# Optimization experiments

Hardware: AMD Instinct MI355X
Metric: run time of the kernel (lower is better)

## Reference

```python
import jax, jax.numpy as jnp
import numpy as np
from math import sqrt

H = 8          # num_heads
ROPE_BASE = 10000.0


def _rotate_half_interleaved(t):
    # rearrange '... (dim r) -> r ... dim' with r=2 then stack [-x2, x1] back interleaved
    x1 = t[..., 0::2]
    x2 = t[..., 1::2]
    return jnp.stack([-x2, x1], axis=-1).reshape(t.shape)


def _apply_rope(t, pos):
    # t: [B,H,L,W] with W even; pos: [L]
    W = t.shape[-1]
    theta = 1.0 / (ROPE_BASE ** (jnp.arange(0, W, 2, dtype=jnp.float32) / W))  # [W/2]
    m_theta = pos[:, None].astype(jnp.float32) * theta[None, :]                 # [L,W/2]
    m_theta = jnp.repeat(m_theta, 2, axis=-1)                                   # [L,W]
    cos = jnp.cos(m_theta)
    sin = jnp.sin(m_theta)
    return cos * t + sin * _rotate_half_interleaved(t)


def setup_inputs() -> dict:
    key = jax.random.key(0)
    ks = jax.random.split(key, 7)
    B, L, D = 2, 2048, 512
    s = 0.05
    return {
        'x': jax.random.normal(ks[0], (B, L, D), jnp.float32),
        'Wq': jax.random.normal(ks[1], (D, D), jnp.float32) * s,
        'bq': jnp.zeros((D,), jnp.float32),
        'Wk': jax.random.normal(ks[2], (D, D), jnp.float32) * s,
        'bk': jnp.zeros((D,), jnp.float32),
        'Wv': jax.random.normal(ks[3], (D, D), jnp.float32) * s,
        'bv': jnp.zeros((D,), jnp.float32),
        'Wo': jax.random.normal(ks[4], (D, D), jnp.float32) * s,
        'bo': jnp.zeros((D,), jnp.float32),
        'bias_emb': jax.random.normal(ks[5], (2, H), jnp.float32) * s,
        'n_vars': 32,
        'n_tokens': 64,
    }


def reference(x, Wq, bq, Wk, bk, Wv, bv, Wo, bo, bias_emb, n_vars, n_tokens):
    B, L, D = x.shape
    E = D // H  # head_dim
    # q/k/v projections (nn.Linear: x @ W.T + b)
    q = (x @ Wq.T + bq).reshape(B, L, H, E).transpose(0, 2, 1, 3)  # [B,H,L,E]
    k = (x @ Wk.T + bk).reshape(B, L, H, E).transpose(0, 2, 1, 3)  # [B,H,L,E]
    v = (x @ Wv.T + bv).reshape(B, L, H, E)                        # [B,S,H,E]

    # partial RoPE on first half of head_dim (partial_factor=(0.0, 0.5))
    half = E // 2
    pos = jnp.arange(L)
    q = jnp.concatenate([_apply_rope(q[..., :half], pos), q[..., half:]], axis=-1)
    k = jnp.concatenate([_apply_rope(k[..., :half], pos), k[..., half:]], axis=-1)

    # binary attention bias by same-variable indicator
    idx = jnp.arange(L)
    vid = idx // n_tokens
    tid = idx % n_tokens
    same_var = vid[:, None] == vid[None, :]                         # [L,L]
    bias = jnp.where(same_var[None], bias_emb[1][:, None, None],
                     bias_emb[0][:, None, None])                    # [H,L,L]

    # TimerCovariateMask: allow same-variable causal; last n_tokens queries
    # may also attend to all earlier keys
    allowed = same_var & (tid[None, :] <= tid[:, None])
    last_rows = idx >= (L - n_tokens)
    early_cols = idx < (L - n_tokens)
    blocked = (~allowed) & ~(last_rows[:, None] & early_cols[None, :])
    attn_mask = jnp.where(blocked[None], -jnp.inf, bias)            # [H,L,L]

    scale = 1.0 / sqrt(E)
    scores = jnp.einsum('bhle,bhse->bhls', q, k) + attn_mask[None]  # [B,H,L,L]
    A = jax.nn.softmax(scale * scores, axis=-1)
    Vout = jnp.einsum('bhls,bshd->blhd', A, v)                      # [B,L,H,E]
    out = Vout.reshape(B, L, H * E) @ Wo.T + bo                     # [B,L,D]
    return out
```

## Files before the change

kernel.cpp:

```cpp
#include <hip/hip_runtime.h>

typedef __attribute__((ext_vector_type(8))) short short8;
typedef __attribute__((ext_vector_type(4))) float f32x4;
typedef __attribute__((ext_vector_type(4))) unsigned short u16x4;

#define MFMA16(a, b, c) __builtin_amdgcn_mfma_f32_16x16x32_bf16(a, b, c, 0, 0, 0)

#define GLD16(gp, lp) __builtin_amdgcn_global_load_lds( \
    (const __attribute__((address_space(1))) unsigned int*)(gp), \
    (__attribute__((address_space(3))) unsigned int*)(lp), 16, 0, 0)

__device__ __forceinline__ unsigned short f2bf(float f) {
    union { float f; unsigned int u; } v; v.f = f;
    unsigned int r = (v.u + 0x7fffu + ((v.u >> 16) & 1u)) >> 16;
    return (unsigned short)r;
}

__global__ __launch_bounds__(256) void convertk(
    const float* __restrict__ x, const float* __restrict__ wq,
    const float* __restrict__ wk, const float* __restrict__ wv,
    const float* __restrict__ wo, unsigned short* __restrict__ xb,
    unsigned short* __restrict__ wb)
{
    int i = (blockIdx.x * 256 + threadIdx.x) * 4;
    const float* src;
    unsigned short* dst;
    if (i < 2097152) { src = x + i; dst = xb + i; }
    else {
        int j = i - 2097152;
        int w = j >> 18;
        int o = j & 262143;
        src = (w == 0 ? wq : w == 1 ? wk : w == 2 ? wv : wo) + o;
        dst = wb + j;
    }
    float4 v = *(const float4*)src;
    u16x4 p;
    p[0] = f2bf(v.x); p[1] = f2bf(v.y); p[2] = f2bf(v.z); p[3] = f2bf(v.w);
    *(u16x4*)dst = p;
}

__global__ __launch_bounds__(256) void gemm_qkv(
    const unsigned short* __restrict__ xb, const unsigned short* __restrict__ wb,
    const float* __restrict__ bq, const float* __restrict__ bk,
    const float* __restrict__ bv,
    unsigned short* __restrict__ qb, unsigned short* __restrict__ kb,
    unsigned short* __restrict__ vT)
{
    const int z = blockIdx.z;
    const unsigned short* Wz = wb + z * 262144;
    const int n0 = blockIdx.x * 128, m0 = blockIdx.y * 64;
    __shared__ unsigned short Al[64 * 32];
    __shared__ unsigned short Bl[128 * 32];
    const int t = threadIdx.x;
    const int lane = t & 63, w = t >> 6;
    const int wrow = (w >> 1) * 32, wcol = (w & 1) * 64;
    const int quad = lane >> 4, n16 = lane & 15;
    const int rA = lane >> 2;
    const int cG = (((lane & 3) ^ ((rA >> 1) & 3))) * 8;
    const int slotq = (quad ^ ((n16 >> 1) & 3)) * 8;
    const int fragA0 = (wrow >> 4) * 512 + n16 * 32 + slotq;
    const int fragB0 = (wcol >> 4) * 512 + n16 * 32 + slotq;
    f32x4 acc[2][4] = {};
    for (int k0 = 0; k0 < 512; k0 += 32) {
        __syncthreads();
        GLD16(&xb[(m0 + w * 16 + rA) * 512 + k0 + cG],      &Al[(w * 16) * 32]);
        GLD16(&Wz[(n0 + w * 32 + rA) * 512 + k0 + cG],      &Bl[(w * 32) * 32]);
        GLD16(&Wz[(n0 + w * 32 + 16 + rA) * 512 + k0 + cG], &Bl[(w * 32 + 16) * 32]);
        __syncthreads();
        short8 af[2], bfr[4];
        #pragma unroll
        for (int i = 0; i < 2; i++) af[i]  = *(const short8*)&Al[fragA0 + i * 512];
        #pragma unroll
        for (int i = 0; i < 4; i++) bfr[i] = *(const short8*)&Bl[fragB0 + i * 512];
        #pragma unroll
        for (int mi = 0; mi < 2; mi++)
            #pragma unroll
            for (int ni = 0; ni < 4; ni++)
                acc[mi][ni] = MFMA16(af[mi], bfr[ni], acc[mi][ni]);
    }
    const float* bias_p = (z == 0) ? bq : (z == 1) ? bk : bv;
    unsigned short* dst01 = (z == 0) ? qb : kb;
    #pragma unroll
    for (int mi = 0; mi < 2; mi++) {
        #pragma unroll
        for (int ni = 0; ni < 4; ni++) {
            const int n = n0 + wcol + ni * 16 + n16;
            const int mb = m0 + wrow + mi * 16 + quad * 4;
            const float bias = bias_p[n];
            const int h = n >> 6;
            const int e_lo = ni * 16 + n16;
            f32x4 v = acc[mi][ni];
            if (z < 2) {
                float vr[4];
                #pragma unroll
                for (int r = 0; r < 4; r++) vr[r] = v[r] + bias;
                if (ni < 2) {
                    const int j = e_lo >> 1;
                    const float theta = exp2f(-(float)j * 0.8304820237218405f);
                    #pragma unroll
                    for (int r = 0; r < 4; r++) {
                        int l = (mb + r) & 2047;
                        float s, c;
                        __sincosf((float)l * theta, &s, &c);
                        float p = __shfl_xor(vr[r], 1);
                        vr[r] = (e_lo & 1) ? (c * vr[r] + s * p) : (c * vr[r] - s * p);
                    }
                }
                #pragma unroll
                for (int r = 0; r < 4; r++) {
                    int m = mb + r, b = m >> 11, l = m & 2047;
                    dst01[((b * 8 + h) * 2048 + l) * 64 + e_lo] = f2bf(vr[r]);
                }
            } else {
                int b = mb >> 11, l = mb & 2047;
                u16x4 pk;
                #pragma unroll
                for (int r = 0; r < 4; r++) pk[r] = f2bf(v[r] + bias);
                *(u16x4*)&vT[((b * 8 + h) * 64 + e_lo) * 2048 + l] = pk;
            }
        }
    }
}

__global__ __launch_bounds__(256) void attn_all(
    const unsigned short* __restrict__ qb, const unsigned short* __restrict__ kb,
    const unsigned short* __restrict__ vT, const float* __restrict__ bias_emb,
    unsigned short* __restrict__ voutb,
    float* __restrict__ Opart, float* __restrict__ Mp, float* __restrict__ Lp)
{
    const int xid = blockIdx.x, h = blockIdx.y, b = blockIdx.z;
    const int t = threadIdx.x, lane = t & 63, w = t >> 6;
    const int quad = lane >> 4, n16 = lane & 15;
    const int bh = b * 8 + h;
    __shared__ unsigned short Pl[4 * 1280];
    unsigned short* Pw = &Pl[w * 1280];
    const int qoff = bh * 2048 * 64;
    const float scale = 0.125f;
    const float bias_same = bias_emb[8 + h];
    const int iloc = w * 16 + quad * 4;

    if (xid < 31) {
        const int var = xid;
        const int m0 = var * 64 + w * 16;
        const int j0 = var * 64;
        short8 aq0 = *(const short8*)&qb[qoff + (m0 + n16) * 64 + quad * 8];
        short8 aq1 = *(const short8*)&qb[qoff + (m0 + n16) * 64 + 32 + quad * 8];
        f32x4 sc[4];
        #pragma unroll
        for (int nt = 0; nt < 4; nt++) {
            short8 k0f = *(const short8*)&kb[qoff + (j0 + nt * 16 + n16) * 64 + quad * 8];
            short8 k1f = *(const short8*)&kb[qoff + (j0 + nt * 16 + n16) * 64 + 32 + quad * 8];
            f32x4 s = {};
            s = MFMA16(aq0, k0f, s);
            s = MFMA16(aq1, k1f, s);
            sc[nt] = s;
        }
        float zl[4][4];
        #pragma unroll
        for (int nt = 0; nt < 4; nt++) {
            int jloc = nt * 16 + n16;
            #pragma unroll
            for (int r = 0; r < 4; r++) {
                float zz = scale * (sc[nt][r] + bias_same);
                if (jloc > iloc + r) zz = -1e30f;
                zl[nt][r] = zz;
            }
        }
        float cm[4], rsum[4], pr[4][4];
        #pragma unroll
        for (int r = 0; r < 4; r++)
            cm[r] = fmaxf(fmaxf(zl[0][r], zl[1][r]), fmaxf(zl[2][r], zl[3][r]));
        #pragma unroll
        for (int off = 1; off < 16; off <<= 1)
            #pragma unroll
            for (int r = 0; r < 4; r++)
                cm[r] = fmaxf(cm[r], __shfl_xor(cm[r], off));
        #pragma unroll
        for (int nt = 0; nt < 4; nt++)
            #pragma unroll
            for (int r = 0; r < 4; r++)
                pr[nt][r] = __expf(zl[nt][r] - cm[r]);
        #pragma unroll
        for (int r = 0; r < 4; r++)
            rsum[r] = (pr[0][r] + pr[1][r]) + (pr[2][r] + pr[3][r]);
        #pragma unroll
        for (int off = 1; off < 16; off <<= 1)
            #pragma unroll
            for (int r = 0; r < 4; r++)
                rsum[r] += __shfl_xor(rsum[r], off);
        #pragma unroll
        for (int nt = 0; nt < 4; nt++) {
            int s = nt >> 1, c = (nt & 1) * 16 + n16;
            #pragma unroll
            for (int r = 0; r < 4; r++)
                Pw[s * 640 + (quad * 4 + r) * 40 + c] = f2bf(pr[nt][r]);
        }
        short8 pa0 = *(const short8*)&Pw[0 * 640 + n16 * 40 + quad * 8];
        short8 pa1 = *(const short8*)&Pw[1 * 640 + n16 * 40 + quad * 8];
        f32x4 oacc[4] = {};
        #pragma unroll
        for (int et = 0; et < 4; et++) {
            const int vrow = (bh * 64 + et * 16 + n16) * 2048;
            short8 v0 = *(const short8*)&vT[vrow + j0 + quad * 8];
            short8 v1 = *(const short8*)&vT[vrow + j0 + 32 + quad * 8];
            oacc[et] = MFMA16(pa0, v0, oacc[et]);
            oacc[et] = MFMA16(pa1, v1, oacc[et]);
        }
        #pragma unroll
        for (int et = 0; et < 4; et++) {
            #pragma unroll
            for (int r = 0; r < 4; r++) {
                float o = oacc[et][r] / rsum[r];
                int l = m0 + quad * 4 + r;
                voutb[(b * 2048 + l) * 512 + h * 64 + et * 16 + n16] = f2bf(o);
            }
        }
    } else {
        const int split = xid - 31;
        const int m0 = 31 * 64 + w * 16;
        const float bias_diff = bias_emb[h];
        short8 aq0 = *(const short8*)&qb[qoff + (m0 + n16) * 64 + quad * 8];
        short8 aq1 = *(const short8*)&qb[qoff + (m0 + n16) * 64 + 32 + quad * 8];
        f32x4 oacc[4] = {};
        float mrow[4], lrow[4];
        #pragma unroll
        for (int r = 0; r < 4; r++) { mrow[r] = -1e30f; lrow[r] = 0.f; }
        #pragma unroll
        for (int ci = 0; ci < 4; ci++) {
            const int chunk = split * 4 + ci;
            const bool diag = (chunk == 31);
            const float biasv = diag ? bias_same : bias_diff;
            const int j0 = chunk * 64;
            f32x4 sc[4];
            #pragma unroll
            for (int nt = 0; nt < 4; nt++) {
                short8 k0f = *(const short8*)&kb[qoff + (j0 + nt * 16 + n16) * 64 + quad * 8];
                short8 k1f = *(const short8*)&kb[qoff + (j0 + nt * 16 + n16) * 64 + 32 + quad * 8];
                f32x4 s = {};
                s = MFMA16(aq0, k0f, s);
                s = MFMA16(aq1, k1f, s);
                sc[nt] = s;
            }
            float zl[4][4];
            #pragma unroll
            for (int nt = 0; nt < 4; nt++) {
                int jloc = nt * 16 + n16;
                #pragma unroll
                for (int r = 0; r < 4; r++) {
                    float zz = scale * (sc[nt][r] + biasv);
                    if (diag && jloc > iloc + r) zz = -1e30f;
                    zl[nt][r] = zz;
                }
            }
            float cm[4];
            #pragma unroll
            for (int r = 0; r < 4; r++)
                cm[r] = fmaxf(fmaxf(zl[0][r], zl[1][r]), fmaxf(zl[2][r], zl[3][r]));
            #pragma unroll
            for (int off = 1; off < 16; off <<= 1)
                #pragma unroll
                for (int r = 0; r < 4; r++)
                    cm[r] = fmaxf(cm[r], __shfl_xor(cm[r], off));
            float mnew[4], alpha[4], rsum[4], pr[4][4];
            #pragma unroll
            for (int r = 0; r < 4; r++) {
                mnew[r] = fmaxf(mrow[r], cm[r]);
                alpha[r] = __expf(mrow[r] - mnew[r]);
            }
            #pragma unroll
            for (int nt = 0; nt < 4; nt++)
                #pragma unroll
                for (int r = 0; r < 4; r++)
                    pr[nt][r] = __expf(zl[nt][r] - mnew[r]);
            #pragma unroll
            for (int r = 0; r < 4; r++)
                rsum[r] = (pr[0][r] + pr[1][r]) + (pr[2][r] + pr[3][r]);
            #pragma unroll
            for (int off = 1; off < 16; off <<= 1)
                #pragma unroll
                for (int r = 0; r < 4; r++)
                    rsum[r] += __shfl_xor(rsum[r], off);
            #pragma unroll
            for (int r = 0; r < 4; r++) {
                lrow[r] = lrow[r] * alpha[r] + rsum[r];
                mrow[r] = mnew[r];
            }
            #pragma unroll
            for (int et = 0; et < 4; et++)
                #pragma unroll
                for (int r = 0; r < 4; r++)
                    oacc[et][r] *= alpha[r];
            #pragma unroll
            for (int nt = 0; nt < 4; nt++) {
                int s = nt >> 1, c = (nt & 1) * 16 + n16;
                #pragma unroll
                for (int r = 0; r < 4; r++)
                    Pw[s * 640 + (quad * 4 + r) * 40 + c] = f2bf(pr[nt][r]);
            }
            short8 pa0 = *(const short8*)&Pw[0 * 640 + n16 * 40 + quad * 8];
            short8 pa1 = *(const short8*)&Pw[1 * 640 + n16 * 40 + quad * 8];
            #pragma unroll
            for (int et = 0; et < 4; et++) {
                const int vrow = (bh * 64 + et * 16 + n16) * 2048;
                short8 v0 = *(const short8*)&vT[vrow + j0 + quad * 8];
                short8 v1 = *(const short8*)&vT[vrow + j0 + 32 + quad * 8];
                oacc[et] = MFMA16(pa0, v0, oacc[et]);
                oacc[et] = MFMA16(pa1, v1, oacc[et]);
            }
        }
        const int pb = (bh * 8 + split) * 64;
        #pragma unroll
        for (int et = 0; et < 4; et++)
            #pragma unroll
            for (int r = 0; r < 4; r++)
                Opart[(pb + w * 16 + quad * 4 + r) * 64 + et * 16 + n16] = oacc[et][r];
        if (n16 == 0) {
            #pragma unroll
            for (int r = 0; r < 4; r++) {
                Mp[pb + w * 16 + quad * 4 + r] = mrow[r];
                Lp[pb + w * 16 + quad * 4 + r] = lrow[r];
            }
        }
    }
}

__global__ __launch_bounds__(256) void attn31_merge(
    const float* __restrict__ Opart, const float* __restrict__ Mp,
    const float* __restrict__ Lp, unsigned short* __restrict__ voutb)
{
    const int bh = blockIdx.x, b = bh >> 3, h = bh & 7;
    const int t = threadIdx.x;
    const int row = t >> 2, c0 = (t & 3) * 16;
    float ms[8];
    float M = -1e30f;
    #pragma unroll
    for (int s = 0; s < 8; s++) {
        ms[s] = Mp[(bh * 8 + s) * 64 + row];
        M = fmaxf(M, ms[s]);
    }
    float L = 0.f;
    float es[8];
    #pragma unroll
    for (int s = 0; s < 8; s++) {
        es[s] = __expf(ms[s] - M);
        L += Lp[(bh * 8 + s) * 64 + row] * es[s];
    }
    float acc[16] = {};
    #pragma unroll
    for (int s = 0; s < 8; s++) {
        const float* op = &Opart[((bh * 8 + s) * 64 + row) * 64 + c0];
        #pragma unroll
        for (int k = 0; k < 4; k++) {
            float4 v = *(const float4*)&op[k * 4];
            acc[k*4+0] += v.x * es[s]; acc[k*4+1] += v.y * es[s];
            acc[k*4+2] += v.z * es[s]; acc[k*4+3] += v.w * es[s];
        }
    }
    const float inv = 1.f / L;
    const int l = 31 * 64 + row;
    u16x4 pk;
    #pragma unroll
    for (int k = 0; k < 4; k++) {
        pk[0] = f2bf(acc[k*4+0] * inv); pk[1] = f2bf(acc[k*4+1] * inv);
        pk[2] = f2bf(acc[k*4+2] * inv); pk[3] = f2bf(acc[k*4+3] * inv);
        *(u16x4*)&voutb[(b * 2048 + l) * 512 + h * 64 + c0 + k * 4] = pk;
    }
}

__global__ __launch_bounds__(256) void gemm_out(
    const unsigned short* __restrict__ ab, const unsigned short* __restrict__ wo,
    const float* __restrict__ bo, float* __restrict__ out)
{
    const int n0 = blockIdx.x * 64, m0 = blockIdx.y * 64;
    __shared__ unsigned short Al[64 * 32];
    __shared__ unsigned short Bl[64 * 32];
    const int t = threadIdx.x;
    const int lane = t & 63, w = t >> 6;
    const int wrow = (w >> 1) * 32, wcol = (w & 1) * 32;
    const int quad = lane >> 4, n16 = lane & 15;
    const int rA = lane >> 2;
    const int cG = (((lane & 3) ^ ((rA >> 1) & 3))) * 8;
    const int slotq = (quad ^ ((n16 >> 1) & 3)) * 8;
    const int fragA0 = (wrow >> 4) * 512 + n16 * 32 + slotq;
    const int fragB0 = (wcol >> 4) * 512 + n16 * 32 + slotq;
    f32x4 acc[2][2] = {};
    for (int k0 = 0; k0 < 512; k0 += 32) {
        __syncthreads();
        GLD16(&ab[(m0 + w * 16 + rA) * 512 + k0 + cG], &Al[(w * 16) * 32]);
        GLD16(&wo[(n0 + w * 16 + rA) * 512 + k0 + cG], &Bl[(w * 16) * 32]);
        __syncthreads();
        short8 af[2], bfr[2];
        #pragma unroll
        for (int i = 0; i < 2; i++) af[i]  = *(const short8*)&Al[fragA0 + i * 512];
        #pragma unroll
        for (int i = 0; i < 2; i++) bfr[i] = *(const short8*)&Bl[fragB0 + i * 512];
        #pragma unroll
        for (int mi = 0; mi < 2; mi++)
            #pragma unroll
            for (int ni = 0; ni < 2; ni++)
                acc[mi][ni] = MFMA16(af[mi], bfr[ni], acc[mi][ni]);
    }
    #pragma unroll
    for (int mi = 0; mi < 2; mi++) {
        #pragma unroll
        for (int ni = 0; ni < 2; ni++) {
            const int n = n0 + wcol + ni * 16 + n16;
            const int mb = m0 + wrow + mi * 16 + quad * 4;
            const float bias = bo[n];
            f32x4 v = acc[mi][ni];
            #pragma unroll
            for (int r = 0; r < 4; r++)
                out[(mb + r) * 512 + n] = v[r] + bias;
        }
    }
}

extern "C" void kernel_launch(void* const* d_in, const int* in_sizes, int n_in,
                              void* d_out, int out_size, void* d_ws, size_t ws_size,
                              hipStream_t stream)
{
    const float* x        = (const float*)d_in[0];
    const float* Wq       = (const float*)d_in[1];
    const float* bq       = (const float*)d_in[2];
    const float* Wk       = (const float*)d_in[3];
    const float* bk       = (const float*)d_in[4];
    const float* Wv       = (const float*)d_in[5];
    const float* bv       = (const float*)d_in[6];
    const float* Wo       = (const float*)d_in[7];
    const float* bo       = (const float*)d_in[8];
    const float* bias_emb = (const float*)d_in[9];

    unsigned short* xb  = (unsigned short*)d_ws;
    unsigned short* wb  = xb + 2097152;
    unsigned short* qb  = wb + 1048576;
    unsigned short* kb  = qb + 2097152;
    unsigned short* vT  = kb + 2097152;
    unsigned short* vob = vT + 2097152;

    float* Opart = (float*)xb;
    float* Mp    = Opart + 524288;
    float* Lp    = Mp + 8192;

    hipLaunchKernelGGL(convertk, dim3(3072), dim3(256), 0, stream,
                       x, Wq, Wk, Wv, Wo, xb, wb);
    hipLaunchKernelGGL(gemm_qkv, dim3(4, 64, 3), dim3(256), 0, stream,
                       xb, wb, bq, bk, bv, qb, kb, vT);
    hipLaunchKernelGGL(attn_all, dim3(39, 8, 2), dim3(256), 0, stream,
                       qb, kb, vT, bias_emb, vob, Opart, Mp, Lp);
    hipLaunchKernelGGL(attn31_merge, dim3(16), dim3(256), 0, stream,
                       Opart, Mp, Lp, vob);
    hipLaunchKernelGGL(gemm_out, dim3(8, 64), dim3(256), 0, stream,
                       vob, wb + 3 * 262144, bo, (float*)d_out);
}
```

Before: 128.1 us.

## Split last-variable attention per chunk, fuse merge via atomic counter, double GEMM K-step

```diff
diff --git a/kernel.cpp b/kernel.cpp
--- a/kernel.cpp
+++ b/kernel.cpp
@@ -20,8 +20,9 @@
     const float* __restrict__ x, const float* __restrict__ wq,
     const float* __restrict__ wk, const float* __restrict__ wv,
     const float* __restrict__ wo, unsigned short* __restrict__ xb,
-    unsigned short* __restrict__ wb)
-{
+    unsigned short* __restrict__ wb, int* __restrict__ cnt)
+{
+    if (blockIdx.x == 0 && threadIdx.x < 16) cnt[threadIdx.x] = 0;
     int i = (blockIdx.x * 256 + threadIdx.x) * 4;
     const float* src;
     unsigned short* dst;
@@ -49,8 +50,8 @@
     const int z = blockIdx.z;
     const unsigned short* Wz = wb + z * 262144;
     const int n0 = blockIdx.x * 128, m0 = blockIdx.y * 64;
-    __shared__ unsigned short Al[64 * 32];
-    __shared__ unsigned short Bl[128 * 32];
+    __shared__ unsigned short Al[8 * 512];
+    __shared__ unsigned short Bl[16 * 512];
     const int t = threadIdx.x;
     const int lane = t & 63, w = t >> 6;
     const int wrow = (w >> 1) * 32, wcol = (w & 1) * 64;
@@ -58,25 +59,34 @@
     const int rA = lane >> 2;
     const int cG = (((lane & 3) ^ ((rA >> 1) & 3))) * 8;
     const int slotq = (quad ^ ((n16 >> 1) & 3)) * 8;
-    const int fragA0 = (wrow >> 4) * 512 + n16 * 32 + slotq;
-    const int fragB0 = (wcol >> 4) * 512 + n16 * 32 + slotq;
     f32x4 acc[2][4] = {};
-    for (int k0 = 0; k0 < 512; k0 += 32) {
+    for (int k0 = 0; k0 < 512; k0 += 64) {
         __syncthreads();
-        GLD16(&xb[(m0 + w * 16 + rA) * 512 + k0 + cG],      &Al[(w * 16) * 32]);
-        GLD16(&Wz[(n0 + w * 32 + rA) * 512 + k0 + cG],      &Bl[(w * 32) * 32]);
-        GLD16(&Wz[(n0 + w * 32 + 16 + rA) * 512 + k0 + cG], &Bl[(w * 32 + 16) * 32]);
+        GLD16(&xb[(m0 + w * 16 + rA) * 512 + k0 + cG],      &Al[(w * 2 + 0) * 512]);
+        GLD16(&xb[(m0 + w * 16 + rA) * 512 + k0 + 32 + cG], &Al[(w * 2 + 1) * 512]);
+        GLD16(&Wz[(n0 + w * 32 + rA) * 512 + k0 + cG],           &Bl[(w * 4 + 0) * 512]);
+        GLD16(&Wz[(n0 + w * 32 + rA) * 512 + k0 + 32 + cG],      &Bl[(w * 4 + 1) * 512]);
+        GLD16(&Wz[(n0 + w * 32 + 16 + rA) * 512 + k0 + cG],      &Bl[(w * 4 + 2) * 512]);
+        GLD16(&Wz[(n0 + w * 32 + 16 + rA) * 512 + k0 + 32 + cG], &Bl[(w * 4 + 3) * 512]);
         __syncthreads();
-        short8 af[2], bfr[4];
-        #pragma unroll
-        for (int i = 0; i < 2; i++) af[i]  = *(const short8*)&Al[fragA0 + i * 512];
-        #pragma unroll
-        for (int i = 0; i < 4; i++) bfr[i] = *(const short8*)&Bl[fragB0 + i * 512];
+        short8 af[2][2], bfr[4][2];
         #pragma unroll
         for (int mi = 0; mi < 2; mi++)
             #pragma unroll
-            for (int ni = 0; ni < 4; ni++)
-                acc[mi][ni] = MFMA16(af[mi], bfr[ni], acc[mi][ni]);
+            for (int p = 0; p < 2; p++)
+                af[mi][p] = *(const short8*)&Al[((2 * (w >> 1) + mi) * 2 + p) * 512 + n16 * 32 + slotq];
+        #pragma unroll
+        for (int ni = 0; ni < 4; ni++)
+            #pragma unroll
+            for (int p = 0; p < 2; p++)
+                bfr[ni][p] = *(const short8*)&Bl[((4 * (w & 1) + ni) * 2 + p) * 512 + n16 * 32 + slotq];
+        #pragma unroll
+        for (int p = 0; p < 2; p++)
+            #pragma unroll
+            for (int mi = 0; mi < 2; mi++)
+                #pragma unroll
+                for (int ni = 0; ni < 4; ni++)
+                    acc[mi][ni] = MFMA16(af[mi][p], bfr[ni][p], acc[mi][ni]);
     }
     const float* bias_p = (z == 0) ? bq : (z == 1) ? bk : bv;
     unsigned short* dst01 = (z == 0) ? qb : kb;
@@ -126,86 +136,92 @@
     const unsigned short* __restrict__ qb, const unsigned short* __restrict__ kb,
     const unsigned short* __restrict__ vT, const float* __restrict__ bias_emb,
     unsigned short* __restrict__ voutb,
-    float* __restrict__ Opart, float* __restrict__ Mp, float* __restrict__ Lp)
+    float* __restrict__ Opart, float* __restrict__ Mp, float* __restrict__ Lp,
+    int* __restrict__ cnt)
 {
     const int xid = blockIdx.x, h = blockIdx.y, b = blockIdx.z;
     const int t = threadIdx.x, lane = t & 63, w = t >> 6;
     const int quad = lane >> 4, n16 = lane & 15;
     const int bh = b * 8 + h;
     __shared__ unsigned short Pl[4 * 1280];
+    __shared__ int mergeflag;
     unsigned short* Pw = &Pl[w * 1280];
     const int qoff = bh * 2048 * 64;
     const float scale = 0.125f;
-    const float bias_same = bias_emb[8 + h];
+    const bool isSplit = (xid >= 31);
+    const int var = isSplit ? 31 : xid;
+    const int chunk = isSplit ? (xid - 31) : xid;
+    const bool causal = (chunk == var);
+    const float biasv = causal ? bias_emb[8 + h] : bias_emb[h];
+    const int m0 = var * 64 + w * 16;
+    const int j0 = chunk * 64;
     const int iloc = w * 16 + quad * 4;
 
-    if (xid < 31) {
-        const int var = xid;
-        const int m0 = var * 64 + w * 16;
-        const int j0 = var * 64;
-        short8 aq0 = *(const short8*)&qb[qoff + (m0 + n16) * 64 + quad * 8];
-        short8 aq1 = *(const short8*)&qb[qoff + (m0 + n16) * 64 + 32 + quad * 8];
-        f32x4 sc[4];
-        #pragma unroll
-        for (int nt = 0; nt < 4; nt++) {
-            short8 k0f = *(const short8*)&kb[qoff + (j0 + nt * 16 + n16) * 64 + quad * 8];
-            short8 k1f = *(const short8*)&kb[qoff + (j0 + nt * 16 + n16) * 64 + 32 + quad * 8];
-            f32x4 s = {};
-            s = MFMA16(aq0, k0f, s);
-            s = MFMA16(aq1, k1f, s);
-            sc[nt] = s;
-        }
-        float zl[4][4];
-        #pragma unroll
-        for (int nt = 0; nt < 4; nt++) {
-            int jloc = nt * 16 + n16;
-            #pragma unroll
-            for (int r = 0; r < 4; r++) {
-                float zz = scale * (sc[nt][r] + bias_same);
-                if (jloc > iloc + r) zz = -1e30f;
-                zl[nt][r] = zz;
-            }
-        }
-        float cm[4], rsum[4], pr[4][4];
-        #pragma unroll
-        for (int r = 0; r < 4; r++)
-            cm[r] = fmaxf(fmaxf(zl[0][r], zl[1][r]), fmaxf(zl[2][r], zl[3][r]));
-        #pragma unroll
-        for (int off = 1; off < 16; off <<= 1)
-            #pragma unroll
-            for (int r = 0; r < 4; r++)
-                cm[r] = fmaxf(cm[r], __shfl_xor(cm[r], off));
-        #pragma unroll
-        for (int nt = 0; nt < 4; nt++)
-            #pragma unroll
-            for (int r = 0; r < 4; r++)
-                pr[nt][r] = __expf(zl[nt][r] - cm[r]);
-        #pragma unroll
-        for (int r = 0; r < 4; r++)
-            rsum[r] = (pr[0][r] + pr[1][r]) + (pr[2][r] + pr[3][r]);
-        #pragma unroll
-        for (int off = 1; off < 16; off <<= 1)
-            #pragma unroll
-            for (int r = 0; r < 4; r++)
-                rsum[r] += __shfl_xor(rsum[r], off);
-        #pragma unroll
-        for (int nt = 0; nt < 4; nt++) {
-            int s = nt >> 1, c = (nt & 1) * 16 + n16;
-            #pragma unroll
-            for (int r = 0; r < 4; r++)
-                Pw[s * 640 + (quad * 4 + r) * 40 + c] = f2bf(pr[nt][r]);
-        }
-        short8 pa0 = *(const short8*)&Pw[0 * 640 + n16 * 40 + quad * 8];
-        short8 pa1 = *(const short8*)&Pw[1 * 640 + n16 * 40 + quad * 8];
-        f32x4 oacc[4] = {};
-        #pragma unroll
-        for (int et = 0; et < 4; et++) {
-            const int vrow = (bh * 64 + et * 16 + n16) * 2048;
-            short8 v0 = *(const short8*)&vT[vrow + j0 + quad * 8];
-            short8 v1 = *(const short8*)&vT[vrow + j0 + 32 + quad * 8];
-            oacc[et] = MFMA16(pa0, v0, oacc[et]);
-            oacc[et] = MFMA16(pa1, v1, oacc[et]);
-        }
+    short8 aq0 = *(const short8*)&qb[qoff + (m0 + n16) * 64 + quad * 8];
+    short8 aq1 = *(const short8*)&qb[qoff + (m0 + n16) * 64 + 32 + quad * 8];
+
+    f32x4 sc[4];
+    #pragma unroll
+    for (int nt = 0; nt < 4; nt++) {
+        short8 k0f = *(const short8*)&kb[qoff + (j0 + nt * 16 + n16) * 64 + quad * 8];
+        short8 k1f = *(const short8*)&kb[qoff + (j0 + nt * 16 + n16) * 64 + 32 + quad * 8];
+        f32x4 s = {};
+        s = MFMA16(aq0, k0f, s);
+        s = MFMA16(aq1, k1f, s);
+        sc[nt] = s;
+    }
+    float zl[4][4];
+    #pragma unroll
+    for (int nt = 0; nt < 4; nt++) {
+        int jloc = nt * 16 + n16;
+        #pragma unroll
+        for (int r = 0; r < 4; r++) {
+            float zz = scale * (sc[nt][r] + biasv);
+            if (causal && jloc > iloc + r) zz = -1e30f;
+            zl[nt][r] = zz;
+        }
+    }
+    float cm[4], rsum[4], pr[4][4];
+    #pragma unroll
+    for (int r = 0; r < 4; r++)
+        cm[r] = fmaxf(fmaxf(zl[0][r], zl[1][r]), fmaxf(zl[2][r], zl[3][r]));
+    #pragma unroll
+    for (int off = 1; off < 16; off <<= 1)
+        #pragma unroll
+        for (int r = 0; r < 4; r++)
+            cm[r] = fmaxf(cm[r], __shfl_xor(cm[r], off));
+    #pragma unroll
+    for (int nt = 0; nt < 4; nt++)
+        #pragma unroll
+        for (int r = 0; r < 4; r++)
+            pr[nt][r] = __expf(zl[nt][r] - cm[r]);
+    #pragma unroll
+    for (int r = 0; r < 4; r++)
+        rsum[r] = (pr[0][r] + pr[1][r]) + (pr[2][r] + pr[3][r]);
+    #pragma unroll
+    for (int off = 1; off < 16; off <<= 1)
+        #pragma unroll
+        for (int r = 0; r < 4; r++)
+            rsum[r] += __shfl_xor(rsum[r], off);
+    #pragma unroll
+    for (int nt = 0; nt < 4; nt++) {
+        int s = nt >> 1, c = (nt & 1) * 16 + n16;
+        #pragma unroll
+        for (int r = 0; r < 4; r++)
+            Pw[s * 640 + (quad * 4 + r) * 40 + c] = f2bf(pr[nt][r]);
+    }
+    short8 pa0 = *(const short8*)&Pw[0 * 640 + n16 * 40 + quad * 8];
+    short8 pa1 = *(const short8*)&Pw[1 * 640 + n16 * 40 + quad * 8];
+    f32x4 oacc[4] = {};
+    #pragma unroll
+    for (int et = 0; et < 4; et++) {
+        const int vrow = (bh * 64 + et * 16 + n16) * 2048;
+        short8 v0 = *(const short8*)&vT[vrow + j0 + quad * 8];
+        short8 v1 = *(const short8*)&vT[vrow + j0 + 32 + quad * 8];
+        oacc[et] = MFMA16(pa0, v0, oacc[et]);
+        oacc[et] = MFMA16(pa1, v1, oacc[et]);
+    }
+    if (!isSplit) {
         #pragma unroll
         for (int et = 0; et < 4; et++) {
             #pragma unroll
@@ -215,145 +231,42 @@
                 voutb[(b * 2048 + l) * 512 + h * 64 + et * 16 + n16] = f2bf(o);
             }
         }
-    } else {
-        const int split = xid - 31;
-        const int m0 = 31 * 64 + w * 16;
-        const float bias_diff = bias_emb[h];
-        short8 aq0 = *(const short8*)&qb[qoff + (m0 + n16) * 64 + quad * 8];
-        short8 aq1 = *(const short8*)&qb[qoff + (m0 + n16) * 64 + 32 + quad * 8];
-        f32x4 oacc[4] = {};
-        float mrow[4], lrow[4];
-        #pragma unroll
-        for (int r = 0; r < 4; r++) { mrow[r] = -1e30f; lrow[r] = 0.f; }
-        #pragma unroll
-        for (int ci = 0; ci < 4; ci++) {
-            const int chunk = split * 4 + ci;
-            const bool diag = (chunk == 31);
-            const float biasv = diag ? bias_same : bias_diff;
-            const int j0 = chunk * 64;
-            f32x4 sc[4];
-            #pragma unroll
-            for (int nt = 0; nt < 4; nt++) {
-                short8 k0f = *(const short8*)&kb[qoff + (j0 + nt * 16 + n16) * 64 + quad * 8];
-                short8 k1f = *(const short8*)&kb[qoff + (j0 + nt * 16 + n16) * 64 + 32 + quad * 8];
-                f32x4 s = {};
-                s = MFMA16(aq0, k0f, s);
-                s = MFMA16(aq1, k1f, s);
-                sc[nt] = s;
-            }
-            float zl[4][4];
-            #pragma unroll
-            for (int nt = 0; nt < 4; nt++) {
-                int jloc = nt * 16 + n16;
-                #pragma unroll
-                for (int r = 0; r < 4; r++) {
-                    float zz = scale * (sc[nt][r] + biasv);
-                    if (diag && jloc > iloc + r) zz = -1e30f;
-                    zl[nt][r] = zz;
-                }
-            }
-            float cm[4];
-            #pragma unroll
-            for (int r = 0; r < 4; r++)
-                cm[r] = fmaxf(fmaxf(zl[0][r], zl[1][r]), fmaxf(zl[2][r], zl[3][r]));
-            #pragma unroll
-            for (int off = 1; off < 16; off <<= 1)
-                #pragma unroll
-                for (int r = 0; r < 4; r++)
-                    cm[r] = fmaxf(cm[r], __shfl_xor(cm[r], off));
-            float mnew[4], alpha[4], rsum[4], pr[4][4];
-            #pragma unroll
-            for (int r = 0; r < 4; r++) {
-                mnew[r] = fmaxf(mrow[r], cm[r]);
-                alpha[r] = __expf(mrow[r] - mnew[r]);
-            }
-            #pragma unroll
-            for (int nt = 0; nt < 4; nt++)
-                #pragma unroll
-                for (int r = 0; r < 4; r++)
-                    pr[nt][r] = __expf(zl[nt][r] - mnew[r]);
-            #pragma unroll
-            for (int r = 0; r < 4; r++)
-                rsum[r] = (pr[0][r] + pr[1][r]) + (pr[2][r] + pr[3][r]);
-            #pragma unroll
-            for (int off = 1; off < 16; off <<= 1)
-                #pragma unroll
-                for (int r = 0; r < 4; r++)
-                    rsum[r] += __shfl_xor(rsum[r], off);
-            #pragma unroll
-            for (int r = 0; r < 4; r++) {
-                lrow[r] = lrow[r] * alpha[r] + rsum[r];
-                mrow[r] = mnew[r];
-            }
-            #pragma unroll
-            for (int et = 0; et < 4; et++)
-                #pragma unroll
-                for (int r = 0; r < 4; r++)
-                    oacc[et][r] *= alpha[r];
-            #pragma unroll
-            for (int nt = 0; nt < 4; nt++) {
-                int s = nt >> 1, c = (nt & 1) * 16 + n16;
-                #pragma unroll
-                for (int r = 0; r < 4; r++)
-                    Pw[s * 640 + (quad * 4 + r) * 40 + c] = f2bf(pr[nt][r]);
-            }
-            short8 pa0 = *(const short8*)&Pw[0 * 640 + n16 * 40 + quad * 8];
-            short8 pa1 = *(const short8*)&Pw[1 * 640 + n16 * 40 + quad * 8];
-            #pragma unroll
-            for (int et = 0; et < 4; et++) {
-                const int vrow = (bh * 64 + et * 16 + n16) * 2048;
-                short8 v0 = *(const short8*)&vT[vrow + j0 + quad * 8];
-                short8 v1 = *(const short8*)&vT[vrow + j0 + 32 + quad * 8];
-                oacc[et] = MFMA16(pa0, v0, oacc[et]);
-                oacc[et] = MFMA16(pa1, v1, oacc[et]);
-            }
-        }
-        const int pb = (bh * 8 + split) * 64;
-        #pragma unroll
-        for (int et = 0; et < 4; et++)
-            #pragma unroll
-            for (int r = 0; r < 4; r++)
-                Opart[(pb + w * 16 + quad * 4 + r) * 64 + et * 16 + n16] = oacc[et][r];
-        if (n16 == 0) {
-            #pragma unroll
-            for (int r = 0; r < 4; r++) {
-                Mp[pb + w * 16 + quad * 4 + r] = mrow[r];
-                Lp[pb + w * 16 + quad * 4 + r] = lrow[r];
-            }
-        }
-    }
-}
-
-__global__ __launch_bounds__(256) void attn31_merge(
-    const float* __restrict__ Opart, const float* __restrict__ Mp,
-    const float* __restrict__ Lp, unsigned short* __restrict__ voutb)
-{
-    const int bh = blockIdx.x, b = bh >> 3, h = bh & 7;
-    const int t = threadIdx.x;
+        return;
+    }
+    const int pb = (bh * 32 + chunk) * 64;
+    #pragma unroll
+    for (int et = 0; et < 4; et++)
+        #pragma unroll
+        for (int r = 0; r < 4; r++)
+            Opart[(pb + w * 16 + quad * 4 + r) * 64 + et * 16 + n16] = oacc[et][r];
+    if (n16 == 0) {
+        #pragma unroll
+        for (int r = 0; r < 4; r++) {
+            Mp[pb + iloc + r] = cm[r];
+            Lp[pb + iloc + r] = rsum[r];
+        }
+    }
+    __threadfence();
+    __syncthreads();
+    if (t == 0) mergeflag = (atomicAdd(&cnt[bh], 1) == 31) ? 1 : 0;
+    __syncthreads();
+    if (mergeflag == 0) return;
+    __threadfence();
     const int row = t >> 2, c0 = (t & 3) * 16;
-    float ms[8];
     float M = -1e30f;
-    #pragma unroll
-    for (int s = 0; s < 8; s++) {
-        ms[s] = Mp[(bh * 8 + s) * 64 + row];
-        M = fmaxf(M, ms[s]);
-    }
+    for (int s = 0; s < 32; s++)
+        M = fmaxf(M, Mp[(bh * 32 + s) * 64 + row]);
     float L = 0.f;
-    float es[8];
-    #pragma unroll
-    for (int s = 0; s < 8; s++) {
-        es[s] = __expf(ms[s] - M);
-        L += Lp[(bh * 8 + s) * 64 + row] * es[s];
-    }
     float acc[16] = {};
-    #pragma unroll
-    for (int s = 0; s < 8; s++) {
-        const float* op = &Opart[((bh * 8 + s) * 64 + row) * 64 + c0];
+    for (int s = 0; s < 32; s++) {
+        const float e = __expf(Mp[(bh * 32 + s) * 64 + row] - M);
+        L += Lp[(bh * 32 + s) * 64 + row] * e;
+        const float* op = &Opart[((bh * 32 + s) * 64 + row) * 64 + c0];
         #pragma unroll
         for (int k = 0; k < 4; k++) {
             float4 v = *(const float4*)&op[k * 4];
-            acc[k*4+0] += v.x * es[s]; acc[k*4+1] += v.y * es[s];
-            acc[k*4+2] += v.z * es[s]; acc[k*4+3] += v.w * es[s];
+            acc[k*4+0] += v.x * e; acc[k*4+1] += v.y * e;
+            acc[k*4+2] += v.z * e; acc[k*4+3] += v.w * e;
         }
     }
     const float inv = 1.f / L;
@@ -372,8 +285,8 @@
     const float* __restrict__ bo, float* __restrict__ out)
 {
     const int n0 = blockIdx.x * 64, m0 = blockIdx.y * 64;
-    __shared__ unsigned short Al[64 * 32];
-    __shared__ unsigned short Bl[64 * 32];
+    __shared__ unsigned short Al[8 * 512];
+    __shared__ unsigned short Bl[8 * 512];
     const int t = threadIdx.x;
     const int lane = t & 63, w = t >> 6;
     const int wrow = (w >> 1) * 32, wcol = (w & 1) * 32;
@@ -381,24 +294,32 @@
     const int rA = lane >> 2;
     const int cG = (((lane & 3) ^ ((rA >> 1) & 3))) * 8;
     const int slotq = (quad ^ ((n16 >> 1) & 3)) * 8;
-    const int fragA0 = (wrow >> 4) * 512 + n16 * 32 + slotq;
-    const int fragB0 = (wcol >> 4) * 512 + n16 * 32 + slotq;
     f32x4 acc[2][2] = {};
-    for (int k0 = 0; k0 < 512; k0 += 32) {
+    for (int k0 = 0; k0 < 512; k0 += 64) {
         __syncthreads();
-        GLD16(&ab[(m0 + w * 16 + rA) * 512 + k0 + cG], &Al[(w * 16) * 32]);
-        GLD16(&wo[(n0 + w * 16 + rA) * 512 + k0 + cG], &Bl[(w * 16) * 32]);
+        GLD16(&ab[(m0 + w * 16 + rA) * 512 + k0 + cG],      &Al[(w * 2 + 0) * 512]);
+        GLD16(&ab[(m0 + w * 16 + rA) * 512 + k0 + 32 + cG], &Al[(w * 2 + 1) * 512]);
+        GLD16(&wo[(n0 + w * 16 + rA) * 512 + k0 + cG],      &Bl[(w * 2 + 0) * 512]);
+        GLD16(&wo[(n0 + w * 16 + rA) * 512 + k0 + 32 + cG], &Bl[(w * 2 + 1) * 512]);
         __syncthreads();
-        short8 af[2], bfr[2];
-        #pragma unroll
-        for (int i = 0; i < 2; i++) af[i]  = *(const short8*)&Al[fragA0 + i * 512];
-        #pragma unroll
-        for (int i = 0; i < 2; i++) bfr[i] = *(const short8*)&Bl[fragB0 + i * 512];
+        short8 af[2][2], bfr[2][2];
         #pragma unroll
         for (int mi = 0; mi < 2; mi++)
             #pragma unroll
-            for (int ni = 0; ni < 2; ni++)
-                acc[mi][ni] = MFMA16(af[mi], bfr[ni], acc[mi][ni]);
+            for (int p = 0; p < 2; p++)
+                af[mi][p] = *(const short8*)&Al[((2 * (w >> 1) + mi) * 2 + p) * 512 + n16 * 32 + slotq];
+        #pragma unroll
+        for (int ni = 0; ni < 2; ni++)
+            #pragma unroll
+            for (int p = 0; p < 2; p++)
+                bfr[ni][p] = *(const short8*)&Bl[((2 * (w & 1) + ni) * 2 + p) * 512 + n16 * 32 + slotq];
+        #pragma unroll
+        for (int p = 0; p < 2; p++)
+            #pragma unroll
+            for (int mi = 0; mi < 2; mi++)
+                #pragma unroll
+                for (int ni = 0; ni < 2; ni++)
+                    acc[mi][ni] = MFMA16(af[mi][p], bfr[ni][p], acc[mi][ni]);
     }
     #pragma unroll
     for (int mi = 0; mi < 2; mi++) {
@@ -437,18 +358,17 @@
     unsigned short* vT  = kb + 2097152;
     unsigned short* vob = vT + 2097152;
 
-    float* Opart = (float*)xb;
-    float* Mp    = Opart + 524288;
-    float* Lp    = Mp + 8192;
+    float* Opart = (float*)(vob + 2097152);
+    float* Mp    = Opart + 2097152;
+    float* Lp    = Mp + 32768;
+    int*   cnt   = (int*)(Lp + 32768);
 
     hipLaunchKernelGGL(convertk, dim3(3072), dim3(256), 0, stream,
-                       x, Wq, Wk, Wv, Wo, xb, wb);
+                       x, Wq, Wk, Wv, Wo, xb, wb, cnt);
     hipLaunchKernelGGL(gemm_qkv, dim3(4, 64, 3), dim3(256), 0, stream,
                        xb, wb, bq, bk, bv, qb, kb, vT);
-    hipLaunchKernelGGL(attn_all, dim3(39, 8, 2), dim3(256), 0, stream,
-                       qb, kb, vT, bias_emb, vob, Opart, Mp, Lp);
-    hipLaunchKernelGGL(attn31_merge, dim3(16), dim3(256), 0, stream,
-                       Opart, Mp, Lp, vob);
+    hipLaunchKernelGGL(attn_all, dim3(63, 8, 2), dim3(256), 0, stream,
+                       qb, kb, vT, bias_emb, vob, Opart, Mp, Lp, cnt);
     hipLaunchKernelGGL(gemm_out, dim3(8, 64), dim3(256), 0, stream,
                        vob, wb + 3 * 262144, bo, (float*)d_out);
 }
```

New measurement: 216.4 us. 1.69x slower.
